# Kernel tuning notes

Hardware: AMD Instinct MI355X
Metric: run time of the kernel (lower is better)

## Reference

```python
import jax, jax.numpy as jnp
import numpy as np

B, N, D, H, O, K, N_USER, C = 1, 4096, 64, 4, 64, 2, 4000, 2


def setup_inputs() -> dict:
    key = jax.random.key(0)
    ks = jax.random.split(key, 7)
    h = jax.random.normal(ks[0], (B, N, D), jnp.float32)
    # dense 0/1 adjacency per heterogeneous kind, with self-loops so no row is empty
    adj = jax.random.randint(ks[1], (K, B, N, N), 0, 2).astype(jnp.float32)
    hadj = jnp.maximum(adj, jnp.eye(N, dtype=jnp.float32))
    s = 1.0 / np.sqrt(D).astype(np.float32)
    w = jax.random.normal(ks[2], (K, H, D, O), jnp.float32) * s
    a_src = jax.random.normal(ks[3], (K, H, O, 1), jnp.float32) * (1.0 / np.sqrt(O).astype(np.float32))
    a_dst = jax.random.normal(ks[4], (K, H, O, 1), jnp.float32) * (1.0 / np.sqrt(O).astype(np.float32))
    fc_w = jax.random.normal(ks[5], (C, O * K), jnp.float32) * (1.0 / np.sqrt(O * K).astype(np.float32))
    fc_b = jnp.zeros((C,), jnp.float32)
    return {"h": h, "hadj": hadj, "w": w, "a_src": a_src, "a_dst": a_dst, "fc_w": fc_w, "fc_b": fc_b}


def _gat(h, adj, w_k, a_src_k, a_dst_k):
    # h: (B,N,D); adj: (B,N,N); w_k: (H,D,O); a_*: (H,O,1)
    h_prime = jnp.einsum('bnf,hfo->bhno', h, w_k)          # (B,H,N,O)
    t = jnp.tanh(h_prime)
    attn_src = jnp.einsum('bhno,hoi->bhni', t, a_src_k)    # (B,H,N,1)
    attn_dst = jnp.einsum('bhno,hoi->bhni', t, a_dst_k)    # (B,H,N,1)
    attn = attn_src + jnp.swapaxes(attn_dst, -1, -2)       # (B,H,N,N) broadcast add
    attn = jnp.where(attn >= 0, attn, 0.2 * attn)          # LeakyReLU(0.2)
    attn = jnp.where(adj[:, None] > 0, attn, -jnp.inf)     # dense mask
    attn = jax.nn.softmax(attn, axis=-1)                   # dropout is a no-op in eval
    out = jnp.einsum('bhnm,bhmo->bhno', attn, h_prime)     # (B,H,N,O)
    return out.mean(axis=1)                                # mean over heads -> (B,N,O)


def reference(h, hadj, w, a_src, a_dst, fc_w, fc_b):
    embs = []
    for k in range(K):  # small fixed loop over heterogeneous node kinds
        x = _gat(h, hadj[k], w[k], a_src[k], a_dst[k])
        embs.append(x[:, :N_USER])
    type_aware = jnp.concatenate(embs, axis=-1)            # (B, N_USER, K*O)
    logits = type_aware @ fc_w.T + fc_b                    # (B, N_USER, C)
    return jax.nn.log_softmax(logits, axis=-1)
```

## Files before the change

kernel.cpp:

```cpp
#include <hip/hip_runtime.h>
#include <math.h>

constexpr int KK = 2;
constexpr int HH = 4;
constexpr int NN = 4096;
constexpr int DD = 64;
constexpr int OO = 64;
constexpr int NU = 4000;
constexpr int CC = 2;
constexpr int JSPLIT = 8;
constexpr int JCHUNK = NN / JSPLIT;
constexpr float LOG2E = 1.44269504088896340736f;

typedef float vf4 __attribute__((ext_vector_type(4)));
typedef float vf2 __attribute__((ext_vector_type(2)));

__device__ __forceinline__ float fexp2(float x) {
#if __has_builtin(__builtin_amdgcn_exp2f)
  return __builtin_amdgcn_exp2f(x);
#else
  return exp2f(x);
#endif
}
__device__ __forceinline__ float frcp(float x) {
#if __has_builtin(__builtin_amdgcn_rcpf)
  return __builtin_amdgcn_rcpf(x);
#else
  return 1.0f / x;
#endif
}
__device__ __forceinline__ float ftanh(float x) {
  float e = fexp2(x * (2.0f * LOG2E));
  return 1.0f - 2.0f * frcp(e + 1.0f);
}

__global__ __launch_bounds__(256) void gat_phase1(
    const float* __restrict__ hsrc, const float* __restrict__ w,
    const float* __restrict__ a_src, const float* __restrict__ a_dst,
    const float* __restrict__ fc_w,
    float* __restrict__ src_s, float* __restrict__ att_d,
    float* __restrict__ att_g0, float* __restrict__ att_g1) {
  const int kh = blockIdx.y;
  const int k = kh >> 2;
  const int i0 = blockIdx.x * 64;
  const int tid = threadIdx.x;

  __shared__ float h_s[DD][68];
  __shared__ float w_s[DD][OO];
  __shared__ float part[4][64][17];

  {
    const vf4* wp = (const vf4*)(w + (size_t)kh * DD * OO);
    vf4* ws4 = (vf4*)w_s;
    for (int t = tid; t < DD * OO / 4; t += 256) ws4[t] = wp[t];
  }
  for (int t = tid; t < 1024; t += 256) {
    const int row = t >> 4;
    const int f4 = (t & 15) * 4;
    vf4 v = *(const vf4*)(hsrc + (size_t)(i0 + row) * DD + f4);
    h_s[f4 + 0][row] = v.x;
    h_s[f4 + 1][row] = v.y;
    h_s[f4 + 2][row] = v.z;
    h_s[f4 + 3][row] = v.w;
  }
  __syncthreads();

  const int og = tid & 15;
  const int rg = tid >> 4;
  const int o0 = og * 4;
  const int r0 = rg * 4;

  float hp[4][4];
#pragma unroll
  for (int j = 0; j < 4; ++j)
#pragma unroll
    for (int u = 0; u < 4; ++u) hp[j][u] = 0.0f;

#pragma unroll 8
  for (int f = 0; f < DD; ++f) {
    vf4 hv = *(const vf4*)&h_s[f][r0];
    vf4 wv = *(const vf4*)&w_s[f][o0];
    hp[0][0] = fmaf(hv.x, wv.x, hp[0][0]);
    hp[0][1] = fmaf(hv.x, wv.y, hp[0][1]);
    hp[0][2] = fmaf(hv.x, wv.z, hp[0][2]);
    hp[0][3] = fmaf(hv.x, wv.w, hp[0][3]);
    hp[1][0] = fmaf(hv.y, wv.x, hp[1][0]);
    hp[1][1] = fmaf(hv.y, wv.y, hp[1][1]);
    hp[1][2] = fmaf(hv.y, wv.z, hp[1][2]);
    hp[1][3] = fmaf(hv.y, wv.w, hp[1][3]);
    hp[2][0] = fmaf(hv.z, wv.x, hp[2][0]);
    hp[2][1] = fmaf(hv.z, wv.y, hp[2][1]);
    hp[2][2] = fmaf(hv.z, wv.z, hp[2][2]);
    hp[2][3] = fmaf(hv.z, wv.w, hp[2][3]);
    hp[3][0] = fmaf(hv.w, wv.x, hp[3][0]);
    hp[3][1] = fmaf(hv.w, wv.y, hp[3][1]);
    hp[3][2] = fmaf(hv.w, wv.z, hp[3][2]);
    hp[3][3] = fmaf(hv.w, wv.w, hp[3][3]);
  }

  float as[4], ad[4], f0[4], f1[4];
#pragma unroll
  for (int u = 0; u < 4; ++u) {
    as[u] = a_src[kh * OO + o0 + u];
    ad[u] = a_dst[kh * OO + o0 + u];
    f0[u] = fc_w[0 * (KK * OO) + k * OO + o0 + u];
    f1[u] = fc_w[1 * (KK * OO) + k * OO + o0 + u];
  }

#pragma unroll
  for (int j = 0; j < 4; ++j) {
    float sp = 0.0f, dp = 0.0f, g0 = 0.0f, g1 = 0.0f;
#pragma unroll
    for (int u = 0; u < 4; ++u) {
      float v = hp[j][u];
      float t = ftanh(v);
      sp = fmaf(t, as[u], sp);
      dp = fmaf(t, ad[u], dp);
      g0 = fmaf(v, f0[u], g0);
      g1 = fmaf(v, f1[u], g1);
    }
    part[0][r0 + j][og] = sp;
    part[1][r0 + j][og] = dp;
    part[2][r0 + j][og] = g0;
    part[3][r0 + j][og] = g1;
  }
  __syncthreads();

  {
    const int val = tid & 3;
    const int j2 = tid >> 2;
    const float* pr = &part[val][j2][0];
    vf4 s0 = *(const vf4*)(pr + 0);
    vf4 s1 = *(const vf4*)(pr + 4);
    vf4 s2 = *(const vf4*)(pr + 8);
    vf4 s3 = *(const vf4*)(pr + 12);
    vf4 t4 = s0 + s1 + s2 + s3;
    float sum = t4.x + t4.y + t4.z + t4.w;
    if (val < 2) sum *= LOG2E;
    float* base = (val == 0) ? src_s : (val == 1) ? att_d
                 : (val == 2) ? att_g0 : att_g1;
    base[kh * NN + i0 + j2] = sum;
  }
}

__global__ __launch_bounds__(256) void gat_phase2(
    const float* __restrict__ adj, const float* __restrict__ src_s,
    const float* __restrict__ att_d, const float* __restrict__ att_g0,
    const float* __restrict__ att_g1, float* __restrict__ P) {
  const int k = blockIdx.y >> 3;
  const int chunk = blockIdx.y & 7;
  const int r0 = blockIdx.x * 16;
  const int tid = threadIdx.x;
  const int wave = tid >> 6;
  const int lane = tid & 63;
  const int row = lane & 15;
  const int jsub = lane >> 4;
  const int i = r0 + row;
  const int j0 = chunk * JCHUNK;

  vf2 sreg2[4];
#pragma unroll
  for (int h = 0; h < 4; ++h) {
    float s = src_s[(k * HH + h) * NN + i];
    sreg2[h].x = s;
    sreg2[h].y = s;
  }

  __shared__ float lds_att[12][JCHUNK];
  {
    const float* planes[3] = {att_d, att_g0, att_g1};
#pragma unroll
    for (int step = 0; step < 6; ++step) {
      const int fi = step * 256 + tid;
      const int v = fi >> 7;
      const int pos = (fi & 127) * 4;
      const int p = v >> 2, h = v & 3;
      vf4 val = *(const vf4*)(planes[p] + (size_t)(k * HH + h) * NN + j0 + pos);
      *(vf4*)&lds_att[v][pos] = val;
    }
  }

  vf2 l2[4], a02[4], a12[4];
#pragma unroll
  for (int h = 0; h < 4; ++h) {
    l2[h] = (vf2)(0.0f);
    a02[h] = (vf2)(0.0f);
    a12[h] = (vf2)(0.0f);
  }

  __syncthreads();

  const float* arow =
      adj + (size_t)k * NN * NN + (size_t)i * NN + j0 + jsub * 4;
  vf4 apre[4];
#pragma unroll
  for (int q = 0; q < 4; ++q)
    apre[q] = *(const vf4*)(arow + (wave + q * 4) * 16);

#pragma unroll
  for (int s = 0; s < 8; ++s) {
    const int t = wave + s * 4;
    const vf4 av = apre[s & 3];
    if (s < 4) apre[s & 3] = *(const vf4*)(arow + (wave + (s + 4) * 4) * 16);
    const int jloc = jsub * 4 + t * 16;
#pragma unroll
    for (int h = 0; h < 4; ++h) {
      vf4 dv = *(const vf4*)&lds_att[0 * 4 + h][jloc];
      vf4 g0v = *(const vf4*)&lds_att[1 * 4 + h][jloc];
      vf4 g1v = *(const vf4*)&lds_att[2 * 4 + h][jloc];
#pragma unroll
      for (int pp = 0; pp < 2; ++pp) {
        vf2 dpair = {dv[2 * pp], dv[2 * pp + 1]};
        vf2 apair = {av[2 * pp], av[2 * pp + 1]};
        vf2 g0p = {g0v[2 * pp], g0v[2 * pp + 1]};
        vf2 g1p = {g1v[2 * pp], g1v[2 * pp + 1]};
        vf2 s2 = sreg2[h] + dpair;
        vf2 sl = __builtin_elementwise_max(s2, s2 * 0.2f);
        vf2 e;
        e.x = fexp2(sl.x);
        e.y = fexp2(sl.y);
        vf2 p2 = apair * e;
        l2[h] += p2;
        a02[h] = __builtin_elementwise_fma(p2, g0p, a02[h]);
        a12[h] = __builtin_elementwise_fma(p2, g1p, a12[h]);
      }
    }
  }

  float l[4], a0[4], a1[4];
#pragma unroll
  for (int h = 0; h < 4; ++h) {
    l[h] = l2[h].x + l2[h].y;
    a0[h] = a02[h].x + a02[h].y;
    a1[h] = a12[h].x + a12[h].y;
    l[h] += __shfl_xor(l[h], 16, 64);
    l[h] += __shfl_xor(l[h], 32, 64);
    a0[h] += __shfl_xor(a0[h], 16, 64);
    a0[h] += __shfl_xor(a0[h], 32, 64);
    a1[h] += __shfl_xor(a1[h], 16, 64);
    a1[h] += __shfl_xor(a1[h], 32, 64);
  }

  __shared__ float sred[4][12][16];
  if (lane < 16) {
#pragma unroll
    for (int h = 0; h < 4; ++h) {
      sred[wave][h * 3 + 0][row] = l[h];
      sred[wave][h * 3 + 1][row] = a0[h];
      sred[wave][h * 3 + 2][row] = a1[h];
    }
  }
  __syncthreads();
  if (tid < 192) {
    const int v = tid >> 4;
    const int rr = tid & 15;
    float sum =
        sred[0][v][rr] + sred[1][v][rr] + sred[2][v][rr] + sred[3][v][rr];
    const int h = v / 3, c = v % 3;
    size_t base =
        ((((size_t)(k * JSPLIT + chunk) * HH + h) * 3 + c)) * NU + (r0 + rr);
    P[base] = sum;
  }
}

__global__ __launch_bounds__(256) void gat_phase3(
    const float* __restrict__ P, const float* __restrict__ fc_b,
    float* __restrict__ out) {
  const int i = blockIdx.x * 256 + threadIdx.x;
  if (i >= NU) return;
  float l0 = fc_b[0], l1 = fc_b[1];
#pragma unroll
  for (int k = 0; k < KK; ++k) {
#pragma unroll
    for (int q = 0; q < HH; ++q) {
      float ls = 0.0f, a0 = 0.0f, a1 = 0.0f;
#pragma unroll
      for (int ch = 0; ch < JSPLIT; ++ch) {
        size_t b = (((size_t)(k * JSPLIT + ch) * HH + q) * 3) * NU + i;
        ls += P[b];
        a0 += P[b + NU];
        a1 += P[b + 2 * (size_t)NU];
      }
      float inv = 1.0f / ls;
      l0 = fmaf(0.25f * a0, inv, l0);
      l1 = fmaf(0.25f * a1, inv, l1);
    }
  }
  float m = fmaxf(l0, l1);
  float lse = m + logf(expf(l0 - m) + expf(l1 - m));
  out[i * CC + 0] = l0 - lse;
  out[i * CC + 1] = l1 - lse;
}

extern "C" void kernel_launch(void* const* d_in, const int* in_sizes, int n_in,
                              void* d_out, int out_size, void* d_ws, size_t ws_size,
                              hipStream_t stream) {
  const float* hsrc  = (const float*)d_in[0];
  const float* hadj  = (const float*)d_in[1];
  const float* w     = (const float*)d_in[2];
  const float* a_src = (const float*)d_in[3];
  const float* a_dst = (const float*)d_in[4];
  const float* fc_w  = (const float*)d_in[5];
  const float* fc_b  = (const float*)d_in[6];
  float* out = (float*)d_out;

  char* ws = (char*)d_ws;
  float* src_s  = (float*)(ws + 0 * 131072);
  float* att_d  = (float*)(ws + 1 * 131072);
  float* att_g0 = (float*)(ws + 2 * 131072);
  float* att_g1 = (float*)(ws + 3 * 131072);
  float* P      = (float*)(ws + 4 * 131072);

  dim3 g1(NN / 64, KK * HH);
  gat_phase1<<<g1, 256, 0, stream>>>(hsrc, w, a_src, a_dst, fc_w,
                                     src_s, att_d, att_g0, att_g1);
  dim3 g2(NU / 16, KK * JSPLIT);
  gat_phase2<<<g2, 256, 0, stream>>>(hadj, src_s, att_d, att_g0, att_g1, P);
  gat_phase3<<<(NU + 255) / 256, 256, 0, stream>>>(P, fc_b, out);
}
```

Before: 225.3 us.

## Factor exponentials out of the attention loop by precomputing per-node exp terms

The change rewrites exp2(LeakyReLU(s+d)) as max(exp2(s)·exp2(d), exp2(0.2s)·exp2(0.2d)). This works because exp is monotonic and LeakyReLU is a max of two linear terms. Phase1 now precomputes the paired exponentials per node and interleaves the g0/g1 values, so the inner loop of phase2 uses multiplies and a max instead of transcendental exp calls. The j-split is also doubled to 16, which adds more blocks and more partial results for phase3 to reduce. The cost is extra precision risk: the products could overflow or underflow if the scores are large, since no max is subtracted.

```diff
diff --git a/kernel.cpp b/kernel.cpp
--- a/kernel.cpp
+++ b/kernel.cpp
@@ -8,7 +8,7 @@
 constexpr int OO = 64;
 constexpr int NU = 4000;
 constexpr int CC = 2;
-constexpr int JSPLIT = 8;
+constexpr int JSPLIT = 16;
 constexpr int JCHUNK = NN / JSPLIT;
 constexpr float LOG2E = 1.44269504088896340736f;
 
@@ -38,8 +38,8 @@
     const float* __restrict__ hsrc, const float* __restrict__ w,
     const float* __restrict__ a_src, const float* __restrict__ a_dst,
     const float* __restrict__ fc_w,
-    float* __restrict__ src_s, float* __restrict__ att_d,
-    float* __restrict__ att_g0, float* __restrict__ att_g1) {
+    float* __restrict__ srcAA, float* __restrict__ bb5,
+    float* __restrict__ gg) {
   const int kh = blockIdx.y;
   const int k = kh >> 2;
   const int i0 = blockIdx.x * 64;
@@ -136,19 +136,27 @@
     vf4 s3 = *(const vf4*)(pr + 12);
     vf4 t4 = s0 + s1 + s2 + s3;
     float sum = t4.x + t4.y + t4.z + t4.w;
-    if (val < 2) sum *= LOG2E;
-    float* base = (val == 0) ? src_s : (val == 1) ? att_d
-                 : (val == 2) ? att_g0 : att_g1;
-    base[kh * NN + i0 + j2] = sum;
+    const size_t idx = (size_t)kh * NN + i0 + j2;
+    if (val == 0) {
+      float sp = sum * LOG2E;
+      vf2 v = {fexp2(sp), fexp2(0.2f * sp)};
+      *(vf2*)(srcAA + idx * 2) = v;
+    } else if (val == 1) {
+      float dp = sum * LOG2E;
+      vf2 v = {fexp2(dp), fexp2(0.2f * dp)};
+      *(vf2*)(bb5 + idx * 2) = v;
+    } else {
+      gg[idx * 2 + (val - 2)] = sum;
+    }
   }
 }
 
 __global__ __launch_bounds__(256) void gat_phase2(
-    const float* __restrict__ adj, const float* __restrict__ src_s,
-    const float* __restrict__ att_d, const float* __restrict__ att_g0,
-    const float* __restrict__ att_g1, float* __restrict__ P) {
-  const int k = blockIdx.y >> 3;
-  const int chunk = blockIdx.y & 7;
+    const float* __restrict__ adj, const float* __restrict__ srcAA,
+    const float* __restrict__ bb5, const float* __restrict__ gg,
+    float* __restrict__ P) {
+  const int k = blockIdx.y >> 4;
+  const int chunk = blockIdx.y & 15;
   const int r0 = blockIdx.x * 16;
   const int tid = threadIdx.x;
   const int wave = tid >> 6;
@@ -158,81 +166,73 @@
   const int i = r0 + row;
   const int j0 = chunk * JCHUNK;
 
-  vf2 sreg2[4];
+  __shared__ float lds_bb[HH][JCHUNK * 2];
+  __shared__ float lds_gg[HH][JCHUNK * 2];
+
+#pragma unroll
+  for (int step = 0; step < 4; ++step) {
+    const int idx = step * 256 + tid;
+    const int sel = idx >> 9;
+    const int h = (idx >> 7) & 3;
+    const int pos = (idx & 127) * 4;
+    const float* src =
+        (sel ? gg : bb5) + ((size_t)(k * HH + h) * NN + j0) * 2 + pos;
+    vf4 v = *(const vf4*)src;
+    if (sel)
+      *(vf4*)&lds_gg[h][pos] = v;
+    else
+      *(vf4*)&lds_bb[h][pos] = v;
+  }
+
+  vf2 AA[4];
+#pragma unroll
+  for (int h = 0; h < 4; ++h)
+    AA[h] = *(const vf2*)(srcAA + ((size_t)(k * HH + h) * NN + i) * 2);
+
+  float l[4], a0[4], a1[4];
 #pragma unroll
   for (int h = 0; h < 4; ++h) {
-    float s = src_s[(k * HH + h) * NN + i];
-    sreg2[h].x = s;
-    sreg2[h].y = s;
-  }
-
-  __shared__ float lds_att[12][JCHUNK];
-  {
-    const float* planes[3] = {att_d, att_g0, att_g1};
-#pragma unroll
-    for (int step = 0; step < 6; ++step) {
-      const int fi = step * 256 + tid;
-      const int v = fi >> 7;
-      const int pos = (fi & 127) * 4;
-      const int p = v >> 2, h = v & 3;
-      vf4 val = *(const vf4*)(planes[p] + (size_t)(k * HH + h) * NN + j0 + pos);
-      *(vf4*)&lds_att[v][pos] = val;
-    }
-  }
-
-  vf2 l2[4], a02[4], a12[4];
-#pragma unroll
-  for (int h = 0; h < 4; ++h) {
-    l2[h] = (vf2)(0.0f);
-    a02[h] = (vf2)(0.0f);
-    a12[h] = (vf2)(0.0f);
+    l[h] = 0.0f;
+    a0[h] = 0.0f;
+    a1[h] = 0.0f;
   }
 
   __syncthreads();
 
   const float* arow =
       adj + (size_t)k * NN * NN + (size_t)i * NN + j0 + jsub * 4;
-  vf4 apre[4];
+  vf4 aj[4];
 #pragma unroll
   for (int q = 0; q < 4; ++q)
-    apre[q] = *(const vf4*)(arow + (wave + q * 4) * 16);
-
-#pragma unroll
-  for (int s = 0; s < 8; ++s) {
+    aj[q] = *(const vf4*)(arow + (wave + q * 4) * 16);
+
+#pragma unroll
+  for (int s = 0; s < 4; ++s) {
     const int t = wave + s * 4;
-    const vf4 av = apre[s & 3];
-    if (s < 4) apre[s & 3] = *(const vf4*)(arow + (wave + (s + 4) * 4) * 16);
-    const int jloc = jsub * 4 + t * 16;
+    const vf4 av = aj[s];
+    const int jl = (t * 16 + jsub * 4) * 2;
 #pragma unroll
     for (int h = 0; h < 4; ++h) {
-      vf4 dv = *(const vf4*)&lds_att[0 * 4 + h][jloc];
-      vf4 g0v = *(const vf4*)&lds_att[1 * 4 + h][jloc];
-      vf4 g1v = *(const vf4*)&lds_att[2 * 4 + h][jloc];
-#pragma unroll
-      for (int pp = 0; pp < 2; ++pp) {
-        vf2 dpair = {dv[2 * pp], dv[2 * pp + 1]};
-        vf2 apair = {av[2 * pp], av[2 * pp + 1]};
-        vf2 g0p = {g0v[2 * pp], g0v[2 * pp + 1]};
-        vf2 g1p = {g1v[2 * pp], g1v[2 * pp + 1]};
-        vf2 s2 = sreg2[h] + dpair;
-        vf2 sl = __builtin_elementwise_max(s2, s2 * 0.2f);
-        vf2 e;
-        e.x = fexp2(sl.x);
-        e.y = fexp2(sl.y);
-        vf2 p2 = apair * e;
-        l2[h] += p2;
-        a02[h] = __builtin_elementwise_fma(p2, g0p, a02[h]);
-        a12[h] = __builtin_elementwise_fma(p2, g1p, a12[h]);
+      vf4 b01 = *(const vf4*)&lds_bb[h][jl];
+      vf4 b23 = *(const vf4*)&lds_bb[h][jl + 4];
+      vf4 g01 = *(const vf4*)&lds_gg[h][jl];
+      vf4 g23 = *(const vf4*)&lds_gg[h][jl + 4];
+      vf2 bp[4] = {{b01.x, b01.y}, {b01.z, b01.w}, {b23.x, b23.y}, {b23.z, b23.w}};
+      vf2 gp[4] = {{g01.x, g01.y}, {g01.z, g01.w}, {g23.x, g23.y}, {g23.z, g23.w}};
+#pragma unroll
+      for (int jj = 0; jj < 4; ++jj) {
+        vf2 PP = AA[h] * bp[jj];
+        float e = fmaxf(PP.x, PP.y);
+        float pa = e * av[jj];
+        l[h] += pa;
+        a0[h] = fmaf(pa, gp[jj].x, a0[h]);
+        a1[h] = fmaf(pa, gp[jj].y, a1[h]);
       }
     }
   }
 
-  float l[4], a0[4], a1[4];
 #pragma unroll
   for (int h = 0; h < 4; ++h) {
-    l[h] = l2[h].x + l2[h].y;
-    a0[h] = a02[h].x + a02[h].y;
-    a1[h] = a12[h].x + a12[h].y;
     l[h] += __shfl_xor(l[h], 16, 64);
     l[h] += __shfl_xor(l[h], 32, 64);
     a0[h] += __shfl_xor(a0[h], 16, 64);
@@ -305,16 +305,15 @@
   float* out = (float*)d_out;
 
   char* ws = (char*)d_ws;
-  float* src_s  = (float*)(ws + 0 * 131072);
-  float* att_d  = (float*)(ws + 1 * 131072);
-  float* att_g0 = (float*)(ws + 2 * 131072);
-  float* att_g1 = (float*)(ws + 3 * 131072);
-  float* P      = (float*)(ws + 4 * 131072);
+  float* srcAA = (float*)(ws + 0);
+  float* bb5   = (float*)(ws + 262144);
+  float* gg    = (float*)(ws + 524288);
+  float* P     = (float*)(ws + 786432);
 
   dim3 g1(NN / 64, KK * HH);
   gat_phase1<<<g1, 256, 0, stream>>>(hsrc, w, a_src, a_dst, fc_w,
-                                     src_s, att_d, att_g0, att_g1);
+                                     srcAA, bb5, gg);
   dim3 g2(NU / 16, KK * JSPLIT);
-  gat_phase2<<<g2, 256, 0, stream>>>(hadj, src_s, att_d, att_g0, att_g1, P);
+  gat_phase2<<<g2, 256, 0, stream>>>(hadj, srcAA, bb5, gg, P);
   gat_phase3<<<(NU + 255) / 256, 256, 0, stream>>>(P, fc_b, out);
 }
```

Measured after the change: 222.0 us. Within noise of the previous version (-1.5%).
